# Kernel tuning notes

Hardware: AMD Instinct MI355X
Metric: run time of the kernel (lower is better)

The kernel has to match this reference:

```python
import jax, jax.numpy as jnp
import numpy as np

D_MODEL = 1024
N_HEADS = 4  # hardcoded in the torch reshape
EPS = 1e-5


def setup_inputs() -> dict:
    key = jax.random.key(0)
    ks = jax.random.split(key, 5)
    d = D_MODEL
    x = jax.random.normal(ks[0], (4, 2048, d), dtype=jnp.float32)
    scale = 1.0 / np.sqrt(d)
    qkv_w = jax.random.normal(ks[1], (3 * d, d), dtype=jnp.float32) * scale
    qkv_b = jnp.zeros((3 * d,), dtype=jnp.float32)
    wo_w = jax.random.normal(ks[2], (d, d), dtype=jnp.float32) * scale
    wo_b = jnp.zeros((d,), dtype=jnp.float32)
    gamma = jnp.ones((d,), dtype=jnp.float32)
    beta = jnp.zeros((d,), dtype=jnp.float32)
    return {"x": x, "qkv_w": qkv_w, "qkv_b": qkv_b, "wo_w": wo_w,
            "wo_b": wo_b, "gamma": gamma, "beta": beta}


def reference(x, qkv_w, qkv_b, wo_w, wo_b, gamma, beta):
    b, s, d = x.shape
    h = N_HEADS
    hd = d // h
    # QKV projection (torch Linear: x @ W.T + b)
    qkv = x @ qkv_w.T + qkv_b                      # [b, s, 3d]
    qkv = qkv.reshape(b, s, 3, h, hd)
    qkv = jnp.transpose(qkv, (2, 0, 3, 1, 4))      # [3, b, h, s, hd]
    q, k, v = qkv[0], qkv[1], qkv[2]
    scores = jnp.einsum('bhqd,bhkd->bhqk', q, k) * (hd ** -0.5)
    attn = jax.nn.softmax(scores, axis=-1)
    out = jnp.einsum('bhqk,bhkd->bhqd', attn, v)   # [b, h, s, hd]
    out = jnp.transpose(out, (0, 2, 1, 3)).reshape(b, s, d)
    y = x + (out @ wo_w.T + wo_b)
    # LayerNorm over last dim
    mu = jnp.mean(y, axis=-1, keepdims=True)
    var = jnp.var(y, axis=-1, keepdims=True)
    return (y - mu) * jax.lax.rsqrt(var + EPS) * gamma + beta
```

## Files before the change

kernel.cpp:

```cpp
#include <hip/hip_runtime.h>
#include <hip/hip_bf16.h>

#define SEQ 2048
#define DM  1024
#define NH  4
#define HD  256

typedef __attribute__((ext_vector_type(4))) float f32x4;
typedef __attribute__((ext_vector_type(16))) float f32x16;
typedef __attribute__((ext_vector_type(8))) short bf16x8;

__device__ __forceinline__ void gload16(const void* g, void* l) {
  __builtin_amdgcn_global_load_lds(
      (__attribute__((address_space(1))) void*)(unsigned long long)(g),
      (__attribute__((address_space(3))) void*)(l), 16, 0, 0);
}

__device__ __forceinline__ bf16x8 ldg8(const __hip_bfloat16* p) {
  return *reinterpret_cast<const bf16x8*>(p);
}

__device__ __forceinline__ unsigned pack2(float a, float b) {
  __hip_bfloat162 t = __float22bfloat162_rn(make_float2(a, b));
  return *reinterpret_cast<unsigned*>(&t);
}

__device__ __forceinline__ short bfbits(float x) {
  __hip_bfloat16 h = __float2bfloat16(x);
  return *reinterpret_cast<short*>(&h);
}

__global__ __launch_bounds__(256) void cvt3(const float* __restrict__ x,
                                            const float* __restrict__ qw,
                                            const float* __restrict__ ww,
                                            __hip_bfloat16* __restrict__ xo,
                                            __hip_bfloat16* __restrict__ qo,
                                            __hip_bfloat16* __restrict__ wo) {
  int i = blockIdx.x * 256 + threadIdx.x;
  const float* src;
  __hip_bfloat16* dst;
  int j;
  if (i < 2097152) {
    src = x; dst = xo; j = i;
  } else if (i < 2883584) {
    src = qw; dst = qo; j = i - 2097152;
  } else {
    src = ww; dst = wo; j = i - 2883584;
  }
  float4 v = reinterpret_cast<const float4*>(src)[j];
  __hip_bfloat162* o2 = reinterpret_cast<__hip_bfloat162*>(dst);
  o2[j * 2 + 0] = __float22bfloat162_rn(make_float2(v.x, v.y));
  o2[j * 2 + 1] = __float22bfloat162_rn(make_float2(v.z, v.w));
}

template <int EPI>
__global__ __launch_bounds__(256, 3) void gemm_bt(
    const __hip_bfloat16* __restrict__ A, const __hip_bfloat16* __restrict__ Bw,
    const float* __restrict__ bias, const float* __restrict__ resid,
    __hip_bfloat16* __restrict__ Cb, float* __restrict__ Cf,
    __hip_bfloat16* __restrict__ vtr, int M, int N, int K) {
  __shared__ __hip_bfloat16 lA[3][128 * 32];
  __shared__ __hip_bfloat16 lB[3][128 * 32];
  const int t = threadIdx.x;
  const int w = t >> 6, l = t & 63;
  const int lg = l >> 4, li = l & 15;
  const int m0 = blockIdx.y * 128, n0 = blockIdx.x * 128;
  const int wm = (w >> 1) * 64, wn = (w & 1) * 64;
  const int ca = (((t & 3) ^ ((t >> 3) & 3))) * 8;
  const __hip_bfloat16* gA0 = A + (size_t)(m0 + (t >> 2)) * K + ca;
  const __hip_bfloat16* gA1 = A + (size_t)(m0 + 64 + (t >> 2)) * K + ca;
  const __hip_bfloat16* gB0 = Bw + (size_t)(n0 + (t >> 2)) * K + ca;
  const __hip_bfloat16* gB1 = Bw + (size_t)(n0 + 64 + (t >> 2)) * K + ca;
  const int loff = t * 8;

  auto STAGE = [&](int kt, int buf) {
    const int k0 = kt * 32;
    gload16(gA0 + k0, &lA[buf][loff]);
    gload16(gA1 + k0, &lA[buf][loff + 2048]);
    gload16(gB0 + k0, &lB[buf][loff]);
    gload16(gB1 + k0, &lB[buf][loff + 2048]);
  };

  f32x4 acc[4][4] = {};
  const int T = K >> 5;
  STAGE(0, 0);
  STAGE(1, 1);
  asm volatile("s_waitcnt vmcnt(4)" ::: "memory");
  __builtin_amdgcn_sched_barrier(0);
  __builtin_amdgcn_s_barrier();
  __builtin_amdgcn_sched_barrier(0);
  int cur = 0, nx2 = 2;
  for (int kt = 0; kt < T; ++kt) {
    if (kt + 2 < T) STAGE(kt + 2, nx2);
    bf16x8 af[4], bfr[4];
#pragma unroll
    for (int i = 0; i < 4; i++) {
      const int row = wm + i * 16 + li;
      af[i] = ldg8(&lA[cur][row * 32 + ((lg ^ ((row >> 1) & 3)) << 3)]);
    }
#pragma unroll
    for (int i = 0; i < 4; i++) {
      const int row = wn + i * 16 + li;
      bfr[i] = ldg8(&lB[cur][row * 32 + ((lg ^ ((row >> 1) & 3)) << 3)]);
    }
    asm volatile("s_waitcnt lgkmcnt(0)" ::: "memory");
    __builtin_amdgcn_sched_barrier(0);
#pragma unroll
    for (int mi = 0; mi < 4; mi++)
#pragma unroll
      for (int ni = 0; ni < 4; ni++)
        acc[mi][ni] = __builtin_amdgcn_mfma_f32_16x16x32_bf16(af[mi], bfr[ni], acc[mi][ni], 0, 0, 0);
    if (kt + 2 < T) {
      asm volatile("s_waitcnt vmcnt(4)" ::: "memory");
    } else {
      asm volatile("s_waitcnt vmcnt(0)" ::: "memory");
    }
    __builtin_amdgcn_sched_barrier(0);
    __builtin_amdgcn_s_barrier();
    __builtin_amdgcn_sched_barrier(0);
    cur = (cur == 2) ? 0 : cur + 1;
    nx2 = (nx2 == 2) ? 0 : nx2 + 1;
  }
#pragma unroll
  for (int ni = 0; ni < 4; ni++) {
    const int col = n0 + wn + ni * 16 + li;
    const float bv = bias[col];
    if (EPI == 0 && col >= 2048) {
      const int hh = (col - 2048) >> 8;
      const int dd = (col - 2048) & 255;
      __hip_bfloat16* vcol =
          vtr + ((size_t)((m0 >> 11) * 4 + hh) * 256 + dd) * 2048 + (m0 & 2047);
#pragma unroll
      for (int mi = 0; mi < 4; mi++) {
        const int off = wm + mi * 16 + lg * 4;
#pragma unroll
        for (int r = 0; r < 4; r++)
          vcol[off + r] = __float2bfloat16(acc[mi][ni][r] + bv);
      }
    } else {
#pragma unroll
      for (int mi = 0; mi < 4; mi++) {
        const int rowb = m0 + wm + mi * 16 + lg * 4;
#pragma unroll
        for (int r = 0; r < 4; r++) {
          const size_t idx = (size_t)(rowb + r) * N + col;
          float v = acc[mi][ni][r] + bv;
          if (EPI) {
            Cf[idx] = v + resid[idx];
          } else {
            Cb[idx] = __float2bfloat16(v);
          }
        }
      }
    }
  }
}

__global__ __launch_bounds__(512, 2) void flash_attn(const __hip_bfloat16* __restrict__ qkv,
                                                     const __hip_bfloat16* __restrict__ vt,
                                                     __hip_bfloat16* __restrict__ attno) {
  __shared__ __hip_bfloat16 ldsK[2][2][32 * 256];
  __shared__ __hip_bfloat16 ldsV[2][2][256 * 32];
  __shared__ float mlx[8][2][32];
  const int tid = threadIdx.x, w = tid >> 6, l = tid & 63;
  const int l31 = l & 31, hi = l >> 5;
  const int g = w >> 2, gt = tid & 255;
  const int bid = blockIdx.x;
  const int bh = (bid & 7) * 2 + ((bid >> 3) & 1);
  const int qt = bid >> 4;
  const int b = bh >> 2, h = bh & 3;
  const int qsub = qt * 128 + (w & 3) * 32;
  const int kvbase = g * 1024;
  bf16x8 bq[16];
  {
    const __hip_bfloat16* Qp = qkv + (size_t)(b * SEQ + qsub + l31) * 3072 + h * HD + hi * 8;
#pragma unroll
    for (int kst = 0; kst < 16; kst++) bq[kst] = ldg8(Qp + kst * 16);
  }
  const int kcd = (gt & 31) ^ ((gt >> 5) & 7);
  const __hip_bfloat16* Kg =
      qkv + (size_t)(b * SEQ + kvbase + (gt >> 5)) * 3072 + 1024 + h * HD + kcd * 8;
  const int vcd = (gt & 3) ^ ((gt >> 3) & 3);
  const __hip_bfloat16* Vg =
      vt + (size_t)bh * HD * SEQ + (size_t)(gt >> 2) * SEQ + kvbase + vcd * 8;
  __hip_bfloat16* lKb[2] = {&ldsK[g][0][0], &ldsK[g][1][0]};
  __hip_bfloat16* lVb[2] = {&ldsV[g][0][0], &ldsV[g][1][0]};

  f32x16 oacc[8] = {};
  float m_run = -1e30f, lsum = 0.f;

#pragma unroll
  for (int i = 0; i < 4; i++) gload16(Kg + (size_t)(i * 8) * 3072, lKb[0] + i * 2048 + gt * 8);
#pragma unroll
  for (int i = 0; i < 4; i++) gload16(Vg + (size_t)(i * 64) * SEQ, lVb[0] + i * 2048 + gt * 8);
  __syncthreads();

#pragma unroll 2
  for (int t = 0; t < 32; ++t) {
    const int cur = t & 1;
    if (t + 1 < 32) {
      const int nk = (t + 1) * 32;
#pragma unroll
      for (int i = 0; i < 4; i++)
        gload16(Kg + (size_t)(nk + i * 8) * 3072, lKb[cur ^ 1] + i * 2048 + gt * 8);
#pragma unroll
      for (int i = 0; i < 4; i++)
        gload16(Vg + (size_t)(i * 64) * SEQ + nk, lVb[cur ^ 1] + i * 2048 + gt * 8);
    }
    const __hip_bfloat16* lK = lKb[cur];
    const __hip_bfloat16* lV = lVb[cur];
    f32x16 sa = {}, sb = {};
    const int ksw = l31 & 7;
    __builtin_amdgcn_s_setprio(1);
#pragma unroll
    for (int kst = 0; kst < 8; kst++) {
      bf16x8 aka = ldg8(&lK[l31 * 256 + (((4 * kst + hi) ^ ksw) << 3)]);
      bf16x8 akb = ldg8(&lK[l31 * 256 + (((4 * kst + 2 + hi) ^ ksw) << 3)]);
      sa = __builtin_amdgcn_mfma_f32_32x32x16_bf16(aka, bq[2 * kst], sa, 0, 0, 0);
      sb = __builtin_amdgcn_mfma_f32_32x32x16_bf16(akb, bq[2 * kst + 1], sb, 0, 0, 0);
    }
    __builtin_amdgcn_s_setprio(0);
#pragma unroll
    for (int r = 0; r < 16; r++) sa[r] = (sa[r] + sb[r]) * 0.0625f;
    float rmax = sa[0];
#pragma unroll
    for (int r = 1; r < 16; r++) rmax = fmaxf(rmax, sa[r]);
    rmax = fmaxf(rmax, __shfl_xor(rmax, 32));
    if (rmax > m_run + 8.f) {
      const float alpha = __expf(m_run - rmax);
      m_run = rmax;
      lsum *= alpha;
#pragma unroll
      for (int dt = 0; dt < 8; dt++)
#pragma unroll
        for (int r = 0; r < 16; r++) oacc[dt][r] *= alpha;
    }
    float psum = 0.f;
#pragma unroll
    for (int r = 0; r < 16; r++) {
      sa[r] = __expf(sa[r] - m_run);
      psum += sa[r];
    }
    lsum += psum + __shfl_xor(psum, 32);
#pragma unroll
    for (int ks = 0; ks < 2; ks++) {
      const int rb = ks * 8;
      unsigned a0 = pack2(sa[rb + 0], sa[rb + 1]);
      unsigned a1 = pack2(sa[rb + 2], sa[rb + 3]);
      unsigned b0 = pack2(sa[rb + 4], sa[rb + 5]);
      unsigned b1 = pack2(sa[rb + 6], sa[rb + 7]);
      unsigned s0 = (unsigned)__shfl_xor((int)(hi ? a0 : b0), 32);
      unsigned s1 = (unsigned)__shfl_xor((int)(hi ? a1 : b1), 32);
      union { unsigned u[4]; bf16x8 v; } pw;
      pw.u[0] = hi ? s0 : a0;
      pw.u[1] = hi ? s1 : a1;
      pw.u[2] = hi ? b0 : s0;
      pw.u[3] = hi ? b1 : s1;
      __builtin_amdgcn_s_setprio(1);
#pragma unroll
      for (int dt = 0; dt < 8; dt++) {
        const int drow = dt * 32 + l31;
        bf16x8 av = ldg8(&lV[drow * 32 + (((ks * 2 + hi) ^ ((drow >> 1) & 3)) << 3)]);
        oacc[dt] = __builtin_amdgcn_mfma_f32_32x32x16_bf16(av, pw.v, oacc[dt], 0, 0, 0);
      }
      __builtin_amdgcn_s_setprio(0);
    }
    __syncthreads();
  }
  if (l < 32) {
    mlx[w][0][l] = m_run;
    mlx[w][1][l] = lsum;
  }
  __syncthreads();
  {
    const float m_o = mlx[w ^ 4][0][l31];
    const float l_o = mlx[w ^ 4][1][l31];
    const float mm = fmaxf(m_run, m_o);
    const float e_s = __expf(m_run - mm), e_o = __expf(m_o - mm);
    const float wgt = e_s / (e_s * lsum + e_o * l_o);
#pragma unroll
    for (int dt = 0; dt < 8; dt++)
#pragma unroll
      for (int r = 0; r < 16; r++) oacc[dt][r] *= wgt;
  }
  const int pair = w & 3;
  float* xch = pair < 2 ? reinterpret_cast<float*>(&ldsK[0][0][0]) + pair * 8192
                        : reinterpret_cast<float*>(&ldsV[0][0][0]) + (pair - 2) * 8192;
  if (g == 0) {
#pragma unroll
    for (int dt = 0; dt < 8; dt++)
#pragma unroll
      for (int rq = 0; rq < 4; rq++) {
        const int dch = dt * 8 + 2 * rq + hi;
        f32x4 v;
#pragma unroll
        for (int i = 0; i < 4; i++) v[i] = oacc[dt][4 * rq + i];
        *reinterpret_cast<f32x4*>(&xch[l31 * 256 + ((dch ^ (l31 & 7)) << 2)]) = v;
      }
  }
  __syncthreads();
  if (g == 1) {
    const size_t rowb = (size_t)(b * SEQ + qsub + l31) * DM + h * HD;
#pragma unroll
    for (int dt = 0; dt < 8; dt++)
#pragma unroll
      for (int rq = 0; rq < 4; rq++) {
        const int dch = dt * 8 + 2 * rq + hi;
        f32x4 p = *reinterpret_cast<const f32x4*>(&xch[l31 * 256 + ((dch ^ (l31 & 7)) << 2)]);
        short4 sv;
        sv.x = bfbits(p[0] + oacc[dt][4 * rq + 0]);
        sv.y = bfbits(p[1] + oacc[dt][4 * rq + 1]);
        sv.z = bfbits(p[2] + oacc[dt][4 * rq + 2]);
        sv.w = bfbits(p[3] + oacc[dt][4 * rq + 3]);
        *reinterpret_cast<short4*>(
            reinterpret_cast<short*>(attno + rowb + dt * 32 + 8 * rq + 4 * hi)) = sv;
      }
  }
}

__global__ __launch_bounds__(256) void layernorm_k(const float* __restrict__ y,
                                                   const float* __restrict__ gamma,
                                                   const float* __restrict__ beta,
                                                   float* __restrict__ out) {
  const int w = threadIdx.x >> 6, l = threadIdx.x & 63;
  const size_t row = (size_t)blockIdx.x * 4 + w;
  const float4* yp = reinterpret_cast<const float4*>(y + row * DM);
  float4 v[4];
  float s = 0.f, s2 = 0.f;
#pragma unroll
  for (int i = 0; i < 4; i++) {
    v[i] = yp[i * 64 + l];
    s += v[i].x + v[i].y + v[i].z + v[i].w;
    s2 += v[i].x * v[i].x + v[i].y * v[i].y + v[i].z * v[i].z + v[i].w * v[i].w;
  }
#pragma unroll
  for (int off = 1; off < 64; off <<= 1) {
    s += __shfl_xor(s, off);
    s2 += __shfl_xor(s2, off);
  }
  const float mu = s * (1.f / 1024.f);
  const float rs = rsqrtf(s2 * (1.f / 1024.f) - mu * mu + 1e-5f);
  const float4* gp = reinterpret_cast<const float4*>(gamma);
  const float4* bp = reinterpret_cast<const float4*>(beta);
  float4* op = reinterpret_cast<float4*>(out + row * DM);
#pragma unroll
  for (int i = 0; i < 4; i++) {
    float4 g = gp[i * 64 + l], bb = bp[i * 64 + l];
    float4 o;
    o.x = (v[i].x - mu) * rs * g.x + bb.x;
    o.y = (v[i].y - mu) * rs * g.y + bb.y;
    o.z = (v[i].z - mu) * rs * g.z + bb.z;
    o.w = (v[i].w - mu) * rs * g.w + bb.w;
    op[i * 64 + l] = o;
  }
}

extern "C" void kernel_launch(void* const* d_in, const int* in_sizes, int n_in,
                              void* d_out, int out_size, void* d_ws, size_t ws_size,
                              hipStream_t stream) {
  const float* x     = (const float*)d_in[0];
  const float* qkv_w = (const float*)d_in[1];
  const float* qkv_b = (const float*)d_in[2];
  const float* wo_w  = (const float*)d_in[3];
  const float* wo_b  = (const float*)d_in[4];
  const float* gamma = (const float*)d_in[5];
  const float* beta  = (const float*)d_in[6];
  float* out = (float*)d_out;
  char* ws = (char*)d_ws;
  __hip_bfloat16* xbf   = (__hip_bfloat16*)(ws);
  __hip_bfloat16* qkvwb = (__hip_bfloat16*)(ws + 16777216);
  __hip_bfloat16* wowb  = (__hip_bfloat16*)(ws + 23068672);
  __hip_bfloat16* qkv   = (__hip_bfloat16*)(ws + 25165824);
  float*          yb    = (float*)(ws + 25165824);
  __hip_bfloat16* vt    = (__hip_bfloat16*)(ws + 75497472);
  __hip_bfloat16* attno = xbf;

  cvt3<<<12288, 256, 0, stream>>>(x, qkv_w, wo_w, xbf, qkvwb, wowb);
  gemm_bt<0><<<dim3(24, 64), 256, 0, stream>>>(xbf, qkvwb, qkv_b, nullptr, qkv, nullptr,
                                               vt, 8192, 3072, 1024);
  flash_attn<<<256, 512, 0, stream>>>(qkv, vt, attno);
  gemm_bt<1><<<dim3(8, 64), 256, 0, stream>>>(attno, wowb, wo_b, x, nullptr, yb,
                                              nullptr, 8192, 1024, 1024);
  layernorm_k<<<2048, 256, 0, stream>>>(yb, gamma, beta, out);
}
```

Before: 230.2 us.

## Drop split-KV in flash attention; one 256-thread block walks all keys

Flash attention previously ran 512-thread blocks in which two wave groups each covered half of the key/value sequence, then merged their softmax statistics and partial outputs through LDS. Now each 256-thread block handles the whole key range itself over twice as many iterations. The output is normalised by 1/lsum and written straight to global memory. This removes the cross-group merge, its extra barriers and half the LDS footprint. The cost is half as many waves per block and a serial KV loop twice as long, which weakens latency hiding on a grid of only 256 blocks.

```diff
diff --git a/kernel.cpp b/kernel.cpp
--- a/kernel.cpp
+++ b/kernel.cpp
@@ -156,59 +156,54 @@
   }
 }
 
-__global__ __launch_bounds__(512, 2) void flash_attn(const __hip_bfloat16* __restrict__ qkv,
+__global__ __launch_bounds__(256, 2) void flash_attn(const __hip_bfloat16* __restrict__ qkv,
                                                      const __hip_bfloat16* __restrict__ vt,
                                                      __hip_bfloat16* __restrict__ attno) {
-  __shared__ __hip_bfloat16 ldsK[2][2][32 * 256];
-  __shared__ __hip_bfloat16 ldsV[2][2][256 * 32];
-  __shared__ float mlx[8][2][32];
+  __shared__ __hip_bfloat16 ldsK[2][32 * 256];
+  __shared__ __hip_bfloat16 ldsV[2][256 * 32];
   const int tid = threadIdx.x, w = tid >> 6, l = tid & 63;
   const int l31 = l & 31, hi = l >> 5;
-  const int g = w >> 2, gt = tid & 255;
   const int bid = blockIdx.x;
   const int bh = (bid & 7) * 2 + ((bid >> 3) & 1);
   const int qt = bid >> 4;
   const int b = bh >> 2, h = bh & 3;
-  const int qsub = qt * 128 + (w & 3) * 32;
-  const int kvbase = g * 1024;
+  const int qsub = qt * 128 + w * 32;
   bf16x8 bq[16];
   {
     const __hip_bfloat16* Qp = qkv + (size_t)(b * SEQ + qsub + l31) * 3072 + h * HD + hi * 8;
 #pragma unroll
     for (int kst = 0; kst < 16; kst++) bq[kst] = ldg8(Qp + kst * 16);
   }
-  const int kcd = (gt & 31) ^ ((gt >> 5) & 7);
+  const int kcd = (tid & 31) ^ ((tid >> 5) & 7);
   const __hip_bfloat16* Kg =
-      qkv + (size_t)(b * SEQ + kvbase + (gt >> 5)) * 3072 + 1024 + h * HD + kcd * 8;
-  const int vcd = (gt & 3) ^ ((gt >> 3) & 3);
+      qkv + (size_t)(b * SEQ + (tid >> 5)) * 3072 + 1024 + h * HD + kcd * 8;
+  const int vcd = (tid & 3) ^ ((tid >> 3) & 3);
   const __hip_bfloat16* Vg =
-      vt + (size_t)bh * HD * SEQ + (size_t)(gt >> 2) * SEQ + kvbase + vcd * 8;
-  __hip_bfloat16* lKb[2] = {&ldsK[g][0][0], &ldsK[g][1][0]};
-  __hip_bfloat16* lVb[2] = {&ldsV[g][0][0], &ldsV[g][1][0]};
+      vt + (size_t)bh * HD * SEQ + (size_t)(tid >> 2) * SEQ + vcd * 8;
 
   f32x16 oacc[8] = {};
   float m_run = -1e30f, lsum = 0.f;
 
 #pragma unroll
-  for (int i = 0; i < 4; i++) gload16(Kg + (size_t)(i * 8) * 3072, lKb[0] + i * 2048 + gt * 8);
-#pragma unroll
-  for (int i = 0; i < 4; i++) gload16(Vg + (size_t)(i * 64) * SEQ, lVb[0] + i * 2048 + gt * 8);
+  for (int i = 0; i < 4; i++) gload16(Kg + (size_t)(i * 8) * 3072, &ldsK[0][i * 2048 + tid * 8]);
+#pragma unroll
+  for (int i = 0; i < 4; i++) gload16(Vg + (size_t)(i * 64) * SEQ, &ldsV[0][i * 2048 + tid * 8]);
   __syncthreads();
 
 #pragma unroll 2
-  for (int t = 0; t < 32; ++t) {
+  for (int t = 0; t < 64; ++t) {
     const int cur = t & 1;
-    if (t + 1 < 32) {
+    if (t + 1 < 64) {
       const int nk = (t + 1) * 32;
 #pragma unroll
       for (int i = 0; i < 4; i++)
-        gload16(Kg + (size_t)(nk + i * 8) * 3072, lKb[cur ^ 1] + i * 2048 + gt * 8);
+        gload16(Kg + (size_t)(nk + i * 8) * 3072, &ldsK[cur ^ 1][i * 2048 + tid * 8]);
 #pragma unroll
       for (int i = 0; i < 4; i++)
-        gload16(Vg + (size_t)(i * 64) * SEQ + nk, lVb[cur ^ 1] + i * 2048 + gt * 8);
-    }
-    const __hip_bfloat16* lK = lKb[cur];
-    const __hip_bfloat16* lV = lVb[cur];
+        gload16(Vg + (size_t)(i * 64) * SEQ + nk, &ldsV[cur ^ 1][i * 2048 + tid * 8]);
+    }
+    const __hip_bfloat16* lK = &ldsK[cur][0];
+    const __hip_bfloat16* lV = &ldsV[cur][0];
     f32x16 sa = {}, sb = {};
     const int ksw = l31 & 7;
     __builtin_amdgcn_s_setprio(1);
@@ -267,55 +262,19 @@
     }
     __syncthreads();
   }
-  if (l < 32) {
-    mlx[w][0][l] = m_run;
-    mlx[w][1][l] = lsum;
-  }
-  __syncthreads();
-  {
-    const float m_o = mlx[w ^ 4][0][l31];
-    const float l_o = mlx[w ^ 4][1][l31];
-    const float mm = fmaxf(m_run, m_o);
-    const float e_s = __expf(m_run - mm), e_o = __expf(m_o - mm);
-    const float wgt = e_s / (e_s * lsum + e_o * l_o);
-#pragma unroll
-    for (int dt = 0; dt < 8; dt++)
-#pragma unroll
-      for (int r = 0; r < 16; r++) oacc[dt][r] *= wgt;
-  }
-  const int pair = w & 3;
-  float* xch = pair < 2 ? reinterpret_cast<float*>(&ldsK[0][0][0]) + pair * 8192
-                        : reinterpret_cast<float*>(&ldsV[0][0][0]) + (pair - 2) * 8192;
-  if (g == 0) {
-#pragma unroll
-    for (int dt = 0; dt < 8; dt++)
-#pragma unroll
-      for (int rq = 0; rq < 4; rq++) {
-        const int dch = dt * 8 + 2 * rq + hi;
-        f32x4 v;
-#pragma unroll
-        for (int i = 0; i < 4; i++) v[i] = oacc[dt][4 * rq + i];
-        *reinterpret_cast<f32x4*>(&xch[l31 * 256 + ((dch ^ (l31 & 7)) << 2)]) = v;
-      }
-  }
-  __syncthreads();
-  if (g == 1) {
-    const size_t rowb = (size_t)(b * SEQ + qsub + l31) * DM + h * HD;
-#pragma unroll
-    for (int dt = 0; dt < 8; dt++)
-#pragma unroll
-      for (int rq = 0; rq < 4; rq++) {
-        const int dch = dt * 8 + 2 * rq + hi;
-        f32x4 p = *reinterpret_cast<const f32x4*>(&xch[l31 * 256 + ((dch ^ (l31 & 7)) << 2)]);
-        short4 sv;
-        sv.x = bfbits(p[0] + oacc[dt][4 * rq + 0]);
-        sv.y = bfbits(p[1] + oacc[dt][4 * rq + 1]);
-        sv.z = bfbits(p[2] + oacc[dt][4 * rq + 2]);
-        sv.w = bfbits(p[3] + oacc[dt][4 * rq + 3]);
-        *reinterpret_cast<short4*>(
-            reinterpret_cast<short*>(attno + rowb + dt * 32 + 8 * rq + 4 * hi)) = sv;
-      }
-  }
+  const float inv = 1.f / lsum;
+  __hip_bfloat16* orow = attno + (size_t)(b * SEQ + qsub + l31) * DM + h * HD + 4 * hi;
+#pragma unroll
+  for (int dt = 0; dt < 8; dt++)
+#pragma unroll
+    for (int j = 0; j < 4; j++) {
+      short4 sv;
+      sv.x = bfbits(oacc[dt][4 * j + 0] * inv);
+      sv.y = bfbits(oacc[dt][4 * j + 1] * inv);
+      sv.z = bfbits(oacc[dt][4 * j + 2] * inv);
+      sv.w = bfbits(oacc[dt][4 * j + 3] * inv);
+      *reinterpret_cast<short4*>(reinterpret_cast<short*>(orow + dt * 32 + 8 * j)) = sv;
+    }
 }
 
 __global__ __launch_bounds__(256) void layernorm_k(const float* __restrict__ y,
@@ -378,7 +337,7 @@
   cvt3<<<12288, 256, 0, stream>>>(x, qkv_w, wo_w, xbf, qkvwb, wowb);
   gemm_bt<0><<<dim3(24, 64), 256, 0, stream>>>(xbf, qkvwb, qkv_b, nullptr, qkv, nullptr,
                                                vt, 8192, 3072, 1024);
-  flash_attn<<<256, 512, 0, stream>>>(qkv, vt, attno);
+  flash_attn<<<256, 256, 0, stream>>>(qkv, vt, attno);
   gemm_bt<1><<<dim3(8, 64), 256, 0, stream>>>(attno, wowb, wo_b, x, nullptr, yb,
                                               nullptr, 8192, 1024, 1024);
   layernorm_k<<<2048, 256, 0, stream>>>(yb, gamma, beta, out);
```

Result: slower. 258.3 us (+12.2%).
